# Kernel tuning notes

Measured on AMD Instinct MI355X. Metric: run time of the kernel, lower is better.

## Reference

```python
import jax, jax.numpy as jnp
import numpy as np

N_NODES = 100000
N_EDGES = 1280000
D_IN = 64
D_HID = 64
D_OUT = 1
N_GRAPHS = 512


def setup_inputs() -> dict:
    key = jax.random.key(0)
    ks = jax.random.split(key, 12)
    x = jax.random.normal(ks[0], (N_NODES, D_IN), dtype=jnp.float32)
    edge_index = jax.random.randint(ks[1], (2, N_EDGES), 0, N_NODES, dtype=jnp.int32)
    batch = jnp.sort(jax.random.randint(ks[2], (N_NODES,), 0, N_GRAPHS, dtype=jnp.int32))
    s = 0.1
    w0 = jax.random.normal(ks[3], (D_IN, D_HID), dtype=jnp.float32) * s
    b0 = jnp.zeros((D_HID,), dtype=jnp.float32)
    w1 = jax.random.normal(ks[4], (D_HID, D_HID), dtype=jnp.float32) * s
    b1 = jnp.zeros((D_HID,), dtype=jnp.float32)
    w2 = jax.random.normal(ks[5], (D_HID, D_HID), dtype=jnp.float32) * s
    b2 = jnp.zeros((D_HID,), dtype=jnp.float32)
    fc_w = jax.random.normal(ks[6], (D_HID, D_OUT), dtype=jnp.float32) * s
    fc_b = jnp.zeros((D_OUT,), dtype=jnp.float32)
    return {"x": x, "edge_index": edge_index, "batch": batch,
            "w0": w0, "b0": b0, "w1": w1, "b1": b1, "w2": w2, "b2": b2,
            "fc_w": fc_w, "fc_b": fc_b}


def _gcn_conv(x, w, b, src, dst):
    # PyG GCNConv: h = x @ W; out_i = sum_j norm_ij * h_j over (A + I), sym norm.
    h = x @ w                                           # [N, H]
    ones = jnp.ones((src.shape[0],), dtype=h.dtype)
    deg = jax.ops.segment_sum(ones, dst, num_segments=N_NODES) + 1.0  # +1 self-loop
    dinv = jax.lax.rsqrt(deg)                           # [N]
    norm = dinv[src] * dinv[dst]                        # [E]
    agg = jax.ops.segment_sum(h[src] * norm[:, None], dst, num_segments=N_NODES)
    agg = agg + h * (dinv * dinv)[:, None]              # self-loop term
    return agg + b


def reference(x, edge_index, batch, w0, b0, w1, b1, w2, b2, fc_w, fc_b):
    src, dst = edge_index[0], edge_index[1]
    # 3 stacked GCNConv + relu (dropout is identity in eval mode)
    h = jax.nn.relu(_gcn_conv(x, w0, b0, src, dst))
    h = jax.nn.relu(_gcn_conv(h, w1, b1, src, dst))
    h = jax.nn.relu(_gcn_conv(h, w2, b2, src, dst))
    # global mean pool per graph
    sums = jax.ops.segment_sum(h, batch, num_segments=N_GRAPHS)        # [G, H]
    cnt = jax.ops.segment_sum(jnp.ones((N_NODES,), h.dtype), batch, num_segments=N_GRAPHS)
    mean = sums / jnp.maximum(cnt, 1.0)[:, None]
    return mean @ fc_w + fc_b                            # [G, 1]
```

## Files before the change

### kernel.cpp

```cpp
#include <hip/hip_runtime.h>
#include <hip/hip_fp16.h>
#include <type_traits>

#define N_NODES 100000
#define N_EDGES 1280000
#define N_GRAPHS 512
#define NBK 196
#define CHUNK 3200
#define NCH 400
#define CAP 8192
#define CAPH 4096
#define GEMM_BLOCKS 391

typedef _Float16 v8h __attribute__((ext_vector_type(8)));
typedef float v4f __attribute__((ext_vector_type(4)));

__device__ inline void fmix_lo(float& acc, unsigned h2, float n) {
    asm volatile("v_fma_mix_f32 %0, %1, %2, %0 op_sel:[0,0,0] op_sel_hi:[1,0,0]"
                 : "+v"(acc) : "v"(h2), "v"(n));
}
__device__ inline void fmix_hi(float& acc, unsigned h2, float n) {
    asm volatile("v_fma_mix_f32 %0, %1, %2, %0 op_sel:[1,0,0] op_sel_hi:[1,0,0]"
                 : "+v"(acc) : "v"(h2), "v"(n));
}


template <typename T, bool FOLD>
__device__ inline void gemm_body(int bid, const T* __restrict__ X,
                                 const float* __restrict__ W,
                                 const float* __restrict__ dinv,
                                 __half* __restrict__ H,
                                 _Float16 (*Wt)[72]) {
    int t = threadIdx.x;
    #pragma unroll
    for (int q = 0; q < 4; q++) {
        int idx = t + q * 256;
        int k = idx >> 4;
        int n0 = (idx & 15) * 4;
        float4 v = ((const float4*)W)[idx];
        Wt[n0 + 0][k] = (_Float16)v.x;
        Wt[n0 + 1][k] = (_Float16)v.y;
        Wt[n0 + 2][k] = (_Float16)v.z;
        Wt[n0 + 3][k] = (_Float16)v.w;
    }
    __syncthreads();

    int wv = t >> 6, lane = t & 63;
    int m = lane & 15, quad = lane >> 4;

    v8h bf[4][2];
    #pragma unroll
    for (int c = 0; c < 4; c++)
        #pragma unroll
        for (int h = 0; h < 2; h++)
            bf[c][h] = *(const v8h*)&Wt[c * 16 + m][h * 32 + quad * 8];

    int base = bid * 256 + wv * 64;
    #pragma unroll
    for (int tt = 0; tt < 4; tt++) {
        int tile = base + tt * 16;
        int rA = min(tile + m, N_NODES - 1);
        v8h a0, a1;
        if constexpr (std::is_same<T, float>::value) {
            const float* xp = (const float*)X + (size_t)rA * 64 + quad * 8;
            float4 p0 = *(const float4*)xp;
            float4 p1 = *(const float4*)(xp + 4);
            float4 p2 = *(const float4*)(xp + 32);
            float4 p3 = *(const float4*)(xp + 36);
            a0 = (v8h){(_Float16)p0.x, (_Float16)p0.y, (_Float16)p0.z, (_Float16)p0.w,
                       (_Float16)p1.x, (_Float16)p1.y, (_Float16)p1.z, (_Float16)p1.w};
            a1 = (v8h){(_Float16)p2.x, (_Float16)p2.y, (_Float16)p2.z, (_Float16)p2.w,
                       (_Float16)p3.x, (_Float16)p3.y, (_Float16)p3.z, (_Float16)p3.w};
        } else {
            const _Float16* xp = (const _Float16*)X + (size_t)rA * 64 + quad * 8;
            a0 = *(const v8h*)xp;
            a1 = *(const v8h*)(xp + 32);
        }
        v4f acc[4];
        #pragma unroll
        for (int c = 0; c < 4; c++) {
            acc[c] = (v4f){0.f, 0.f, 0.f, 0.f};
            acc[c] = __builtin_amdgcn_mfma_f32_16x16x32_f16(a0, bf[c][0], acc[c], 0, 0, 0);
            acc[c] = __builtin_amdgcn_mfma_f32_16x16x32_f16(a1, bf[c][1], acc[c], 0, 0, 0);
        }
        #pragma unroll
        for (int r = 0; r < 4; r++) {
            int row = tile + quad * 4 + r;
            if (row < N_NODES) {
                float dv = FOLD ? dinv[row] : 1.0f;
                __half* hp = H + (size_t)row * 64 + m;
                #pragma unroll
                for (int c = 0; c < 4; c++)
                    hp[c * 16] = __float2half(FOLD ? acc[c][r] * dv : acc[c][r]);
            }
        }
    }
}

template <typename T, bool FOLD>
__global__ __launch_bounds__(256) void gemm_mfma(const T* __restrict__ X,
                                                 const float* __restrict__ W,
                                                 const float* __restrict__ dinv,
                                                 __half* __restrict__ H) {
    __shared__ _Float16 Wt[64][72];
    gemm_body<T, FOLD>(blockIdx.x, X, W, dinv, H, Wt);
}


#define SC_BUF   0
#define SC_LCNT  (CHUNK * 4)
#define SC_LLOC  (SC_LCNT + NBK * 4)
#define SC_LCUR  (SC_LLOC + NBK * 4)
#define SC_S     (SC_LCUR + NBK * 4)
#define SC_BYTES (SC_S + 256 * 4)

__global__ __launch_bounds__(256) void scatter_gemm(const int* __restrict__ src,
                                                    const int* __restrict__ dst,
                                                    int* __restrict__ bcur,
                                                    unsigned* __restrict__ pairs,
                                                    const float* __restrict__ x,
                                                    const float* __restrict__ w0,
                                                    __half* __restrict__ H) {
    alignas(16) __shared__ char smem[SC_BYTES];
    if (blockIdx.x >= NCH) {
        gemm_body<float, false>(blockIdx.x - NCH, x, w0, nullptr, H,
                                (_Float16(*)[72])smem);
        return;
    }
    unsigned* buf  = (unsigned*)(smem + SC_BUF);
    int*      lcnt = (int*)(smem + SC_LCNT);
    int*      lloc = (int*)(smem + SC_LLOC);
    int*      lcur = (int*)(smem + SC_LCUR);
    int*      s    = (int*)(smem + SC_S);
    int t = threadIdx.x;
    for (int k = t; k < NBK; k += 256) { lcnt[k] = 0; lcur[k] = 0; }
    __syncthreads();
    int e0 = blockIdx.x * CHUNK;
    for (int i = t; i < CHUNK; i += 256) atomicAdd(&lcnt[dst[e0 + i] >> 9], 1);
    __syncthreads();
    {
        int v = (t < NBK) ? lcnt[t] : 0;
        s[t] = v; __syncthreads();
        for (int d = 1; d < 256; d <<= 1) {
            int xx = (t >= d) ? s[t - d] : 0;
            __syncthreads();
            s[t] += xx;
            __syncthreads();
        }
        if (t < NBK) lloc[t] = s[t] - v;
    }
    __syncthreads();
    for (int i = t; i < CHUNK; i += 256) {
        int d = dst[e0 + i];
        int k = d >> 9;
        int li = lloc[k] + atomicAdd(&lcur[k], 1);
        buf[li] = ((unsigned)src[e0 + i] << 9) | (unsigned)(d & 511);
    }
    __syncthreads();
    for (int k = t; k < NBK; k += 256) {
        int c = lcnt[k];
        if (c) {
            int g = atomicAdd(&bcur[k * 16], c);
            int lo = lloc[k];
            unsigned* dstp = pairs + (size_t)k * CAP;
            for (int j = 0; j < c; j++)
                if (g + j < CAP) dstp[g + j] = buf[lo + j];
        }
    }
}


__global__ __launch_bounds__(256) void bucket_place(const unsigned* __restrict__ pairs,
                                                    const int* __restrict__ bcur,
                                                    int* __restrict__ offs,
                                                    float* __restrict__ dinv,
                                                    int* __restrict__ csr) {
    __shared__ int lcnt[256], lofs[256], lcur[256], red[256];
    __shared__ int lsrc[CAPH];
    int t = threadIdx.x;
    int bb = blockIdx.x;
    int b = bb >> 1, half = bb & 1;
    int node0 = (b << 9) + (half << 8);
    int nn = min(256, N_NODES - node0);
    red[t] = (t < b) ? min(bcur[t * 16], CAP) : 0;
    __syncthreads();
    for (int d = 128; d > 0; d >>= 1) {
        if (t < d) red[t] += red[t + d];
        __syncthreads();
    }
    int bbase = red[0];
    int cnt = min(bcur[b * 16], CAP);
    __syncthreads();
    lcnt[t] = 0; lcur[t] = 0;
    __syncthreads();
    const unsigned* prs = pairs + (size_t)b * CAP;
    for (int i = t; i < cnt; i += 256) {
        int n = prs[i] & 511;
        if ((n >> 8) == half) atomicAdd(&lcnt[n & 255], 1);
    }
    __syncthreads();
    int deg = lcnt[t];
    red[t] = deg; __syncthreads();
    for (int d = 1; d < 256; d <<= 1) {
        int xx = (t >= d) ? red[t - d] : 0;
        __syncthreads();
        red[t] += xx;
        __syncthreads();
    }
    lofs[t] = red[t] - deg;
    int total = red[255];
    int beg = bbase + (half ? (cnt - total) : 0);
    if (t < nn) {
        offs[node0 + t] = beg + lofs[t];
        dinv[node0 + t] = 1.0f / sqrtf((float)deg + 1.0f);
    }
    __syncthreads();
    for (int i = t; i < cnt; i += 256) {
        unsigned pr = prs[i];
        int n = pr & 511;
        if ((n >> 8) == half) {
            int li = lofs[n & 255] + atomicAdd(&lcur[n & 255], 1);
            if (li < CAPH) lsrc[li] = (int)(pr >> 9);
        }
    }
    __syncthreads();
    for (int j = t; j < total; j += 256) csr[beg + j] = lsrc[j];
    if (bb == 0 && t == 0) offs[N_NODES] = N_EDGES;
}


template <bool FULL>
__device__ inline void agg_body(const uint2* __restrict__ Hh, int wid, int lane,
                                const int* __restrict__ offs,
                                const int* __restrict__ csr,
                                const float* __restrict__ dinv,
                                float4& out) {
    int eg = lane >> 4;
    int fq = lane & 15;
    int beg = offs[wid], end = offs[wid + 1];
    float di = dinv[wid];
    uint2 us = Hh[wid * 16 + fq];

    float4 a0 = {0.f, 0.f, 0.f, 0.f};
    float4 a1 = {0.f, 0.f, 0.f, 0.f};
    for (int base = beg; base < end; base += 16) {
        int i0 = base + eg;
        int r0 = csr[i0], r1 = csr[i0 + 4], r2 = csr[i0 + 8], r3 = csr[i0 + 12];
        bool p0 = i0      < end, p1 = i0 + 4  < end,
             p2 = i0 + 8  < end, p3 = i0 + 12 < end;
        int s0 = p0 ? r0 : 0, s1 = p1 ? r1 : 0,
            s2 = p2 ? r2 : 0, s3 = p3 ? r3 : 0;
        uint2 u0 = Hh[(s0 << 4) + fq];
        uint2 u1 = Hh[(s1 << 4) + fq];
        uint2 u2 = Hh[(s2 << 4) + fq];
        uint2 u3 = Hh[(s3 << 4) + fq];
        float n0, n1, n2, n3;
        if constexpr (FULL) {
            float d0 = dinv[s0], d1 = dinv[s1], d2 = dinv[s2], d3 = dinv[s3];
            n0 = p0 ? d0 * di : 0.f;
            n1 = p1 ? d1 * di : 0.f;
            n2 = p2 ? d2 * di : 0.f;
            n3 = p3 ? d3 * di : 0.f;
        } else {
            n0 = p0 ? di : 0.f;
            n1 = p1 ? di : 0.f;
            n2 = p2 ? di : 0.f;
            n3 = p3 ? di : 0.f;
        }
        fmix_lo(a0.x, u0.x, n0); fmix_hi(a0.y, u0.x, n0);
        fmix_lo(a0.z, u0.y, n0); fmix_hi(a0.w, u0.y, n0);
        fmix_lo(a1.x, u1.x, n1); fmix_hi(a1.y, u1.x, n1);
        fmix_lo(a1.z, u1.y, n1); fmix_hi(a1.w, u1.y, n1);
        fmix_lo(a0.x, u2.x, n2); fmix_hi(a0.y, u2.x, n2);
        fmix_lo(a0.z, u2.y, n2); fmix_hi(a0.w, u2.y, n2);
        fmix_lo(a1.x, u3.x, n3); fmix_hi(a1.y, u3.x, n3);
        fmix_lo(a1.z, u3.y, n3); fmix_hi(a1.w, u3.y, n3);
    }
    a0.x += a1.x; a0.y += a1.y; a0.z += a1.z; a0.w += a1.w;
    a0.x += __shfl_xor(a0.x, 16); a0.y += __shfl_xor(a0.y, 16);
    a0.z += __shfl_xor(a0.z, 16); a0.w += __shfl_xor(a0.w, 16);
    a0.x += __shfl_xor(a0.x, 32); a0.y += __shfl_xor(a0.y, 32);
    a0.z += __shfl_xor(a0.z, 32); a0.w += __shfl_xor(a0.w, 32);
    float2 s01 = __half22float2(*(__half2*)&us.x);
    float2 s23 = __half22float2(*(__half2*)&us.y);
    float sw = FULL ? di * di : di;
    out.x = a0.x + s01.x * sw; out.y = a0.y + s01.y * sw;
    out.z = a0.z + s23.x * sw; out.w = a0.w + s23.y * sw;
}

template <bool FULL>
__global__ __launch_bounds__(256) void agg_gcn(const __half* __restrict__ H,
                                               const int* __restrict__ offs,
                                               const int* __restrict__ csr,
                                               const float* __restrict__ dinv,
                                               const float* __restrict__ bias,
                                               __half* __restrict__ Out) {
    int wid = (blockIdx.x * 256 + threadIdx.x) >> 6;
    int lane = threadIdx.x & 63;
    if (wid >= N_NODES) return;
    float4 r;
    agg_body<FULL>((const uint2*)H, wid, lane, offs, csr, dinv, r);
    int fq = lane & 15;
    if ((lane >> 4) == 0) {
        float4 b4 = ((const float4*)bias)[fq];
        __half2 h01 = __float22half2_rn(make_float2(fmaxf(r.x + b4.x, 0.f),
                                                    fmaxf(r.y + b4.y, 0.f)));
        __half2 h23 = __float22half2_rn(make_float2(fmaxf(r.z + b4.z, 0.f),
                                                    fmaxf(r.w + b4.w, 0.f)));
        uint2 u;
        u.x = *(unsigned int*)&h01;
        u.y = *(unsigned int*)&h23;
        ((uint2*)Out)[(size_t)wid * 16 + fq] = u;
    }
}

__global__ __launch_bounds__(256) void agg_gcn_pool(const __half* __restrict__ H,
                                                    const int* __restrict__ offs,
                                                    const int* __restrict__ csr,
                                                    const float* __restrict__ dinv,
                                                    const float* __restrict__ bias,
                                                    const float* __restrict__ fcw,
                                                    float* __restrict__ p) {
    int wid = (blockIdx.x * 256 + threadIdx.x) >> 6;
    int lane = threadIdx.x & 63;
    if (wid >= N_NODES) return;
    float4 r;
    agg_body<false>((const uint2*)H, wid, lane, offs, csr, dinv, r);
    int fq = lane & 15;
    float4 b4 = ((const float4*)bias)[fq];
    float4 f4 = ((const float4*)fcw)[fq];
    float v = fmaxf(r.x + b4.x, 0.f) * f4.x + fmaxf(r.y + b4.y, 0.f) * f4.y
            + fmaxf(r.z + b4.z, 0.f) * f4.z + fmaxf(r.w + b4.w, 0.f) * f4.w;
    v += __shfl_xor(v, 1); v += __shfl_xor(v, 2);
    v += __shfl_xor(v, 4); v += __shfl_xor(v, 8);
    if (lane == 0) p[wid] = v;
}


__device__ inline int lower_bound_batch(const int* __restrict__ batch, int key) {
    int lo = 0, hi = N_NODES;
    while (lo < hi) {
        int mid = (lo + hi) >> 1;
        if (batch[mid] < key) lo = mid + 1; else hi = mid;
    }
    return lo;
}

__global__ __launch_bounds__(256) void graph_reduce(const float* __restrict__ p,
                                                    const int* __restrict__ batch,
                                                    const float* __restrict__ fcb,
                                                    float* __restrict__ out) {
    __shared__ float red[4];
    int g = blockIdx.x;
    int s0 = lower_bound_batch(batch, g);
    int s1 = lower_bound_batch(batch, g + 1);
    float acc = 0.f;
    for (int i = s0 + threadIdx.x; i < s1; i += 256) acc += p[i];
    #pragma unroll
    for (int o = 32; o > 0; o >>= 1) acc += __shfl_xor(acc, o);
    int lane = threadIdx.x & 63, wv = threadIdx.x >> 6;
    if (lane == 0) red[wv] = acc;
    __syncthreads();
    if (threadIdx.x == 0) {
        float sum = red[0] + red[1] + red[2] + red[3];
        out[g] = sum / fmaxf((float)(s1 - s0), 1.f) + fcb[0];
    }
}


extern "C" void kernel_launch(void* const* d_in, const int* in_sizes, int n_in,
                              void* d_out, int out_size, void* d_ws, size_t ws_size,
                              hipStream_t stream) {
    const float* x    = (const float*)d_in[0];
    const int*   ei   = (const int*)d_in[1];
    const int*   batch= (const int*)d_in[2];
    const float* w0   = (const float*)d_in[3];
    const float* b0   = (const float*)d_in[4];
    const float* w1   = (const float*)d_in[5];
    const float* b1   = (const float*)d_in[6];
    const float* w2   = (const float*)d_in[7];
    const float* b2   = (const float*)d_in[8];
    const float* fcw  = (const float*)d_in[9];
    const float* fcb  = (const float*)d_in[10];
    float* out = (float*)d_out;

    const int* src_e = ei;
    const int* dst_e = ei + N_EDGES;

    char* w = (char*)d_ws;
    size_t o = 0;
    int*      bcur = (int*)(w + o);      o += 256 * 16 * 4;
    int*      offs = (int*)(w + o);      o += (size_t)(N_NODES + 8) * 4;
    float*    dinv = (float*)(w + o);    o += (size_t)N_NODES * 4;
    unsigned* pairs= (unsigned*)(w + o); o += (size_t)NBK * CAP * 4;
    int*      csr  = (int*)(w + o);      o += (size_t)(N_EDGES + 16) * 4;
    __half*   bufA = (__half*)(w + o);   o += (size_t)N_NODES * 64 * 2;
    __half*   bufB = (__half*)(w + o);   o += (size_t)N_NODES * 64 * 2;
    float*    pvec = (float*)(w + o);    o += (size_t)N_NODES * 4;

    hipMemsetAsync(bcur, 0, 256 * 16 * 4, stream);

    const int AGG_BLOCKS = N_NODES / 4;

    scatter_gemm<<<NCH + GEMM_BLOCKS, 256, 0, stream>>>(src_e, dst_e, bcur, pairs,
                                                        x, w0, bufA);
    bucket_place<<<2 * NBK, 256, 0, stream>>>(pairs, bcur, offs, dinv, csr);

    agg_gcn<true><<<AGG_BLOCKS, 256, 0, stream>>>(bufA, offs, csr, dinv, b0, bufB);

    gemm_mfma<__half, true><<<GEMM_BLOCKS, 256, 0, stream>>>(bufB, w1, dinv, bufA);
    agg_gcn<false><<<AGG_BLOCKS, 256, 0, stream>>>(bufA, offs, csr, dinv, b1, bufB);

    gemm_mfma<__half, true><<<GEMM_BLOCKS, 256, 0, stream>>>(bufB, w2, dinv, bufA);
    agg_gcn_pool<<<AGG_BLOCKS, 256, 0, stream>>>(bufA, offs, csr, dinv, b2, fcw, pvec);

    graph_reduce<<<N_GRAPHS, 256, 0, stream>>>(pvec, batch, fcb, out);
}
```

Baseline: 291.8 us.

## Pad per-node CSR rows to 16 with sentinel node and vectorize index loads

Each node's neighbour list is padded to a multiple of 16 using a sentinel node index, which points to a zeroed feature row and a zero dinv entry. Each bucket half now writes into its own fixed-stride CSR region, so the cross-bucket prefix sum goes away and per-node end offsets are stored explicitly. The aggregation loop loads four indices at once with an int4 read and drops the bounds predicates and masking, and the destination-degree scaling moves to a single multiply at the end. In exchange, the padded slots cost extra gathers of the zero row, the workspace grows, and any bucket half whose padded size exceeds CSTRIDE gets truncated.

After: 296.7 us. Within noise of the previous version (+1.7%).

```diff
diff --git a/kernel.cpp b/kernel.cpp
--- a/kernel.cpp
+++ b/kernel.cpp
@@ -9,7 +9,7 @@
 #define CHUNK 3200
 #define NCH 400
 #define CAP 8192
-#define CAPH 4096
+#define CSTRIDE 6144
 #define GEMM_BLOCKS 391
 
 typedef _Float16 v8h __attribute__((ext_vector_type(8)));
@@ -173,24 +173,16 @@
 __global__ __launch_bounds__(256) void bucket_place(const unsigned* __restrict__ pairs,
                                                     const int* __restrict__ bcur,
                                                     int* __restrict__ offs,
+                                                    int* __restrict__ dege,
                                                     float* __restrict__ dinv,
                                                     int* __restrict__ csr) {
-    __shared__ int lcnt[256], lofs[256], lcur[256], red[256];
-    __shared__ int lsrc[CAPH];
+    __shared__ int lcnt[256], lofs[256], lcur[256], s[256];
+    __shared__ int lsrc[CSTRIDE];
     int t = threadIdx.x;
     int bb = blockIdx.x;
     int b = bb >> 1, half = bb & 1;
     int node0 = (b << 9) + (half << 8);
-    int nn = min(256, N_NODES - node0);
-    red[t] = (t < b) ? min(bcur[t * 16], CAP) : 0;
-    __syncthreads();
-    for (int d = 128; d > 0; d >>= 1) {
-        if (t < d) red[t] += red[t + d];
-        __syncthreads();
-    }
-    int bbase = red[0];
     int cnt = min(bcur[b * 16], CAP);
-    __syncthreads();
     lcnt[t] = 0; lcur[t] = 0;
     __syncthreads();
     const unsigned* prs = pairs + (size_t)b * CAP;
@@ -200,73 +192,69 @@
     }
     __syncthreads();
     int deg = lcnt[t];
-    red[t] = deg; __syncthreads();
+    int degp = (deg + 15) & ~15;
+    s[t] = degp; __syncthreads();
     for (int d = 1; d < 256; d <<= 1) {
-        int xx = (t >= d) ? red[t - d] : 0;
+        int xx = (t >= d) ? s[t - d] : 0;
         __syncthreads();
-        red[t] += xx;
+        s[t] += xx;
         __syncthreads();
     }
-    lofs[t] = red[t] - deg;
-    int total = red[255];
-    int beg = bbase + (half ? (cnt - total) : 0);
-    if (t < nn) {
-        offs[node0 + t] = beg + lofs[t];
+    int lo = s[t] - degp;
+    int totp = s[255];
+    lofs[t] = lo;
+    int base = bb * CSTRIDE;
+    if (node0 + t < N_NODES) {
+        offs[node0 + t] = base + min(lo, CSTRIDE);
+        dege[node0 + t] = base + min(lo + degp, CSTRIDE);
         dinv[node0 + t] = 1.0f / sqrtf((float)deg + 1.0f);
     }
+    int fillN = min(totp, CSTRIDE);
+    for (int j = t; j < fillN; j += 256) lsrc[j] = N_NODES;
     __syncthreads();
     for (int i = t; i < cnt; i += 256) {
         unsigned pr = prs[i];
         int n = pr & 511;
         if ((n >> 8) == half) {
             int li = lofs[n & 255] + atomicAdd(&lcur[n & 255], 1);
-            if (li < CAPH) lsrc[li] = (int)(pr >> 9);
-        }
-    }
-    __syncthreads();
-    for (int j = t; j < total; j += 256) csr[beg + j] = lsrc[j];
-    if (bb == 0 && t == 0) offs[N_NODES] = N_EDGES;
+            if (li < CSTRIDE) lsrc[li] = (int)(pr >> 9);
+        }
+    }
+    __syncthreads();
+    for (int j = t; j < fillN; j += 256) csr[base + j] = lsrc[j];
+    if (bb == 0 && t == 0) dinv[N_NODES] = 0.f;
 }
 
 
 template <bool FULL>
-__device__ inline void agg_body(const uint2* __restrict__ Hh, int wid, int lane,
+__device__ inline void agg_body(const char* __restrict__ Hb, int wid, int lane,
                                 const int* __restrict__ offs,
+                                const int* __restrict__ dege,
                                 const int* __restrict__ csr,
                                 const float* __restrict__ dinv,
                                 float4& out) {
     int eg = lane >> 4;
     int fq = lane & 15;
-    int beg = offs[wid], end = offs[wid + 1];
+    unsigned fqo = (unsigned)(fq << 3);
+    int beg = offs[wid], end = dege[wid];
     float di = dinv[wid];
-    uint2 us = Hh[wid * 16 + fq];
+    uint2 us = *(const uint2*)(Hb + (((unsigned)wid << 7) | fqo));
+    const char* csrB = (const char*)csr;
 
     float4 a0 = {0.f, 0.f, 0.f, 0.f};
     float4 a1 = {0.f, 0.f, 0.f, 0.f};
-    for (int base = beg; base < end; base += 16) {
-        int i0 = base + eg;
-        int r0 = csr[i0], r1 = csr[i0 + 4], r2 = csr[i0 + 8], r3 = csr[i0 + 12];
-        bool p0 = i0      < end, p1 = i0 + 4  < end,
-             p2 = i0 + 8  < end, p3 = i0 + 12 < end;
-        int s0 = p0 ? r0 : 0, s1 = p1 ? r1 : 0,
-            s2 = p2 ? r2 : 0, s3 = p3 ? r3 : 0;
-        uint2 u0 = Hh[(s0 << 4) + fq];
-        uint2 u1 = Hh[(s1 << 4) + fq];
-        uint2 u2 = Hh[(s2 << 4) + fq];
-        uint2 u3 = Hh[(s3 << 4) + fq];
-        float n0, n1, n2, n3;
-        if constexpr (FULL) {
-            float d0 = dinv[s0], d1 = dinv[s1], d2 = dinv[s2], d3 = dinv[s3];
-            n0 = p0 ? d0 * di : 0.f;
-            n1 = p1 ? d1 * di : 0.f;
-            n2 = p2 ? d2 * di : 0.f;
-            n3 = p3 ? d3 * di : 0.f;
-        } else {
-            n0 = p0 ? di : 0.f;
-            n1 = p1 ? di : 0.f;
-            n2 = p2 ? di : 0.f;
-            n3 = p3 ? di : 0.f;
-        }
+    unsigned ub = (unsigned)((beg + (eg << 2)) << 2);
+    unsigned ue = (unsigned)(end << 2);
+    for (; ub < ue; ub += 64) {
+        int4 cs = *(const int4*)(csrB + ub);
+        uint2 u0 = *(const uint2*)(Hb + (((unsigned)cs.x << 7) | fqo));
+        uint2 u1 = *(const uint2*)(Hb + (((unsigned)cs.y << 7) | fqo));
+        uint2 u2 = *(const uint2*)(Hb + (((unsigned)cs.z << 7) | fqo));
+        uint2 u3 = *(const uint2*)(Hb + (((unsigned)cs.w << 7) | fqo));
+        float n0 = FULL ? dinv[cs.x] : 1.0f;
+        float n1 = FULL ? dinv[cs.y] : 1.0f;
+        float n2 = FULL ? dinv[cs.z] : 1.0f;
+        float n3 = FULL ? dinv[cs.w] : 1.0f;
         fmix_lo(a0.x, u0.x, n0); fmix_hi(a0.y, u0.x, n0);
         fmix_lo(a0.z, u0.y, n0); fmix_hi(a0.w, u0.y, n0);
         fmix_lo(a1.x, u1.x, n1); fmix_hi(a1.y, u1.x, n1);
@@ -283,14 +271,17 @@
     a0.z += __shfl_xor(a0.z, 32); a0.w += __shfl_xor(a0.w, 32);
     float2 s01 = __half22float2(*(__half2*)&us.x);
     float2 s23 = __half22float2(*(__half2*)&us.y);
-    float sw = FULL ? di * di : di;
-    out.x = a0.x + s01.x * sw; out.y = a0.y + s01.y * sw;
-    out.z = a0.z + s23.x * sw; out.w = a0.w + s23.y * sw;
+    float sw = FULL ? di : 1.0f;
+    out.x = (a0.x + s01.x * sw) * di;
+    out.y = (a0.y + s01.y * sw) * di;
+    out.z = (a0.z + s23.x * sw) * di;
+    out.w = (a0.w + s23.y * sw) * di;
 }
 
 template <bool FULL>
 __global__ __launch_bounds__(256) void agg_gcn(const __half* __restrict__ H,
                                                const int* __restrict__ offs,
+                                               const int* __restrict__ dege,
                                                const int* __restrict__ csr,
                                                const float* __restrict__ dinv,
                                                const float* __restrict__ bias,
@@ -299,7 +290,7 @@
     int lane = threadIdx.x & 63;
     if (wid >= N_NODES) return;
     float4 r;
-    agg_body<FULL>((const uint2*)H, wid, lane, offs, csr, dinv, r);
+    agg_body<FULL>((const char*)H, wid, lane, offs, dege, csr, dinv, r);
     int fq = lane & 15;
     if ((lane >> 4) == 0) {
         float4 b4 = ((const float4*)bias)[fq];
@@ -316,6 +307,7 @@
 
 __global__ __launch_bounds__(256) void agg_gcn_pool(const __half* __restrict__ H,
                                                     const int* __restrict__ offs,
+                                                    const int* __restrict__ dege,
                                                     const int* __restrict__ csr,
                                                     const float* __restrict__ dinv,
                                                     const float* __restrict__ bias,
@@ -325,7 +317,7 @@
     int lane = threadIdx.x & 63;
     if (wid >= N_NODES) return;
     float4 r;
-    agg_body<false>((const uint2*)H, wid, lane, offs, csr, dinv, r);
+    agg_body<false>((const char*)H, wid, lane, offs, dege, csr, dinv, r);
     int fq = lane & 15;
     float4 b4 = ((const float4*)bias)[fq];
     float4 f4 = ((const float4*)fcw)[fq];
@@ -391,28 +383,30 @@
     size_t o = 0;
     int*      bcur = (int*)(w + o);      o += 256 * 16 * 4;
     int*      offs = (int*)(w + o);      o += (size_t)(N_NODES + 8) * 4;
-    float*    dinv = (float*)(w + o);    o += (size_t)N_NODES * 4;
+    int*      dege = (int*)(w + o);      o += (size_t)(N_NODES + 8) * 4;
+    float*    dinv = (float*)(w + o);    o += (size_t)(N_NODES + 8) * 4;
     unsigned* pairs= (unsigned*)(w + o); o += (size_t)NBK * CAP * 4;
-    int*      csr  = (int*)(w + o);      o += (size_t)(N_EDGES + 16) * 4;
-    __half*   bufA = (__half*)(w + o);   o += (size_t)N_NODES * 64 * 2;
+    int*      csr  = (int*)(w + o);      o += (size_t)2 * NBK * CSTRIDE * 4;
+    __half*   bufA = (__half*)(w + o);   o += (size_t)(N_NODES + 1) * 64 * 2;
     __half*   bufB = (__half*)(w + o);   o += (size_t)N_NODES * 64 * 2;
     float*    pvec = (float*)(w + o);    o += (size_t)N_NODES * 4;
 
     hipMemsetAsync(bcur, 0, 256 * 16 * 4, stream);
+    hipMemsetAsync(bufA + (size_t)N_NODES * 64, 0, 128, stream);
 
     const int AGG_BLOCKS = N_NODES / 4;
 
     scatter_gemm<<<NCH + GEMM_BLOCKS, 256, 0, stream>>>(src_e, dst_e, bcur, pairs,
                                                         x, w0, bufA);
-    bucket_place<<<2 * NBK, 256, 0, stream>>>(pairs, bcur, offs, dinv, csr);
-
-    agg_gcn<true><<<AGG_BLOCKS, 256, 0, stream>>>(bufA, offs, csr, dinv, b0, bufB);
+    bucket_place<<<2 * NBK, 256, 0, stream>>>(pairs, bcur, offs, dege, dinv, csr);
+
+    agg_gcn<true><<<AGG_BLOCKS, 256, 0, stream>>>(bufA, offs, dege, csr, dinv, b0, bufB);
 
     gemm_mfma<__half, true><<<GEMM_BLOCKS, 256, 0, stream>>>(bufB, w1, dinv, bufA);
-    agg_gcn<false><<<AGG_BLOCKS, 256, 0, stream>>>(bufA, offs, csr, dinv, b1, bufB);
+    agg_gcn<false><<<AGG_BLOCKS, 256, 0, stream>>>(bufA, offs, dege, csr, dinv, b1, bufB);
 
     gemm_mfma<__half, true><<<GEMM_BLOCKS, 256, 0, stream>>>(bufB, w2, dinv, bufA);
-    agg_gcn_pool<<<AGG_BLOCKS, 256, 0, stream>>>(bufA, offs, csr, dinv, b2, fcw, pvec);
+    agg_gcn_pool<<<AGG_BLOCKS, 256, 0, stream>>>(bufA, offs, dege, csr, dinv, b2, fcw, pvec);
 
     graph_reduce<<<N_GRAPHS, 256, 0, stream>>>(pvec, batch, fcb, out);
 }
```
